# Performance work log

Measured on AMD Instinct MI355X. Metric: run time of the kernel, lower is better.

The kernel has to match this reference:

```python
import jax, jax.numpy as jnp
import numpy as np

N = 40000   # input nodes
M = 40000   # output nodes
DEG = 16    # fixed degree -> row_splits = arange(M+1)*DEG
E = M * DEG
B = 2
C = 128     # out_channels == feature channels
H = 128     # hidden_dim
P = 3       # positional dim per node (in_channels)


def setup_inputs() -> dict:
    key = jax.random.key(0)
    k = jax.random.split(key, 8)
    x_in = jax.random.normal(k[0], (N, P), dtype=jnp.float32)
    x_out = jax.random.normal(k[1], (M, P), dtype=jnp.float32)
    in_features = jax.random.normal(k[2], (B, N, C), dtype=jnp.float32)
    neighbor_idx = jax.random.randint(k[3], (E,), 0, N)
    row_splits = jnp.arange(M + 1, dtype=jnp.int32) * DEG
    W1 = jax.random.normal(k[4], (2 * P, H), dtype=jnp.float32) / np.sqrt(2 * P)
    b1 = jnp.zeros((H,), dtype=jnp.float32)
    W2 = jax.random.normal(k[5], (H, C), dtype=jnp.float32) / np.sqrt(H)
    b2 = jnp.zeros((C,), dtype=jnp.float32)
    return {"x_in": x_in, "x_out": x_out, "in_features": in_features,
            "neighbor_idx": neighbor_idx, "row_splits": row_splits,
            "W1": W1, "b1": b1, "W2": W2, "b2": b2}


def reference(x_in, x_out, in_features, neighbor_idx, row_splits, W1, b1, W2, b2):
    e = neighbor_idx.shape[0]
    m = row_splits.shape[0] - 1
    num_reps = row_splits[1:] - row_splits[:-1]               # [M]
    rep_feats = x_in[neighbor_idx]                            # [E, P] gather source coords
    gathered = in_features[:, neighbor_idx]                   # [B, E, C]
    self_feats = jnp.repeat(x_out, num_reps, axis=0, total_repeat_length=e)  # [E, P]
    agg = jnp.concatenate([rep_feats, self_feats], axis=1)    # [E, 2P]
    h = jax.nn.gelu(agg @ W1 + b1, approximate=False)         # torch.nn.GELU = exact erf gelu
    msg = h @ W2 + b2                                         # [E, C]
    weighted = msg[None, :, :] * gathered                     # [B, E, C]
    seg_ids = jnp.repeat(jnp.arange(m), num_reps, total_repeat_length=e)      # [E]
    sums = jax.ops.segment_sum(jnp.transpose(weighted, (1, 0, 2)), seg_ids, num_segments=m)  # [M, B, C]
    counts = jnp.maximum(num_reps, 1).astype(sums.dtype)      # segment_csr 'mean'
    out = sums / counts[:, None, None]                        # [M, B, C]
    return jnp.transpose(out, (1, 0, 2))                      # [B, M, C]
```

## Files before the change

kernel.cpp:

```cpp
#include <hip/hip_runtime.h>
#include <hip/hip_bf16.h>

#define CC 128
#define HH 128
#define NB 8

typedef __attribute__((ext_vector_type(8))) _Float16 half8;
typedef __attribute__((ext_vector_type(2))) _Float16 half2v;
typedef __attribute__((ext_vector_type(2))) __fp16   fp16x2;
typedef __attribute__((ext_vector_type(4))) float f32x4;

union H2U { half2v h; fp16x2 g; unsigned int u; };

__device__ __forceinline__ unsigned int pkrtz(float a, float b) {
    H2U v; v.g = __builtin_amdgcn_cvt_pkrtz(a, b); return v.u;
}

__device__ __forceinline__ float gelu_f(float x) {
    float x2 = x * x;
    float t  = fmaf(0.044715f, x2, 1.0f);
    float a  = x * t;
    float e  = __builtin_amdgcn_exp2f(a * 2.3022092f);
    float r  = __builtin_amdgcn_rcpf(e + 1.0f);
    return fmaf(-x, r, x);
}

__global__ __launch_bounds__(256)
void f32_to_f16_kernel(const float* __restrict__ in,
                       _Float16* __restrict__ out, long n8) {
    long i = (long)blockIdx.x * blockDim.x + threadIdx.x;
    const long stride = (long)gridDim.x * blockDim.x;
    for (; i < n8; i += stride) {
        const float4* p = reinterpret_cast<const float4*>(in) + i * 2;
        float4 a = p[0], b = p[1];
        half8 o;
        o[0] = (_Float16)a.x; o[1] = (_Float16)a.y;
        o[2] = (_Float16)a.z; o[3] = (_Float16)a.w;
        o[4] = (_Float16)b.x; o[5] = (_Float16)b.y;
        o[6] = (_Float16)b.z; o[7] = (_Float16)b.w;
        *reinterpret_cast<half8*>(out + i * 8) = o;
    }
}

template<bool F16G>
__global__ __launch_bounds__(512, 4)
void nmlp_kernel(const float* __restrict__ x_in,
                 const float* __restrict__ x_out,
                 const float* __restrict__ in_feat,
                 const _Float16* __restrict__ gws,
                 const int* __restrict__ nbr,
                 const int* __restrict__ row_splits,
                 const float* __restrict__ W1,
                 const float* __restrict__ b1,
                 const float* __restrict__ W2,
                 const float* __restrict__ b2,
                 float* __restrict__ out,
                 int N, int M)
{
    __shared__ __align__(16) char hb[NB * 16 * 256];
    __shared__ __align__(16) char msgb[NB * 16 * 256];
    __shared__ __align__(16) char aggb[NB * 16 * 16];

    const int tid  = threadIdx.x;
    const int lane = tid & 63;
    const int wave = tid >> 6;
    const int cbase = wave * 16;
    const int l15  = lane & 15;
    const int kgrp = lane >> 4;

    half8 w1frag;
    #pragma unroll
    for (int i = 0; i < 8; ++i) {
        int k = kgrp*8 + i;
        w1frag[i] = (k < 6) ? (_Float16)W1[k*HH + cbase + l15] : (_Float16)0.f;
    }
    half8 bfrag[4];
    #pragma unroll
    for (int kb = 0; kb < 4; ++kb)
        #pragma unroll
        for (int i = 0; i < 8; ++i) {
            int k = kb*32 + kgrp*8 + i;
            bfrag[kb][i] = (_Float16)W2[k*CC + cbase + l15];
        }
    float b1v[4], b2v[4];
    #pragma unroll
    for (int i = 0; i < 4; ++i) {
        b1v[i] = b1[cbase + kgrp*4 + i];
        b2v[i] = b2[cbase + kgrp*4 + i];
    }

    const _Float16* g0p = gws;
    const _Float16* g1p = gws + (size_t)N * CC;
    const float* f0p = in_feat;
    const float* f1p = in_feat + (size_t)N * CC;

    const int arow_off = l15 * 256;
    const int aswz = (l15 & 7) << 4;
    const int wcol_off = (cbase + kgrp*4) * 2;

    const int bb     = lane >> 5;
    const int ehalf  = (lane >> 4) & 1;
    const int cchunk = lane & 15;
    const _Float16* gpb = bb ? g1p : g0p;

    const int ngroups = (M + NB - 1) / NB;
    for (int g = blockIdx.x; g < ngroups; g += gridDim.x) {
        const int m0 = g * NB;
        const int mw = m0 + wave;

        int sW = 0, dgv = 0;
        if (mw < M) { sW = row_splits[mw]; dgv = row_splits[mw+1] - sW; }
        const int dgs = __builtin_amdgcn_readfirstlane(dgv);
        int ids8[8];
        if (dgs == 16 && ((sW & 3) == 0)) {
            const int4 ia = *reinterpret_cast<const int4*>(nbr + sW + ehalf*8);
            const int4 ib = *reinterpret_cast<const int4*>(nbr + sW + ehalf*8 + 4);
            ids8[0]=ia.x; ids8[1]=ia.y; ids8[2]=ia.z; ids8[3]=ia.w;
            ids8[4]=ib.x; ids8[5]=ib.y; ids8[6]=ib.z; ids8[7]=ib.w;
        } else {
            #pragma unroll
            for (int e8 = 0; e8 < 8; ++e8) {
                const int e = ehalf*8 + e8;
                ids8[e8] = (e < dgs) ? nbr[sW + e] : 0;
            }
        }
        uint4 gv[8];
        if (F16G) {
            const _Float16* gcp = gpb + cchunk*8;
            #pragma unroll
            for (int e8 = 0; e8 < 8; ++e8)
                gv[e8] = *reinterpret_cast<const uint4*>(
                    gcp + (size_t)ids8[e8]*CC);
        }

        if (tid < NB*16) {
            const int r = tid >> 4, e = tid & 15;
            const int m = m0 + r;
            int id = 0; int dg = 0;
            if (m < M) { int s = row_splits[m]; dg = row_splits[m+1] - s;
                         if (e < dg) id = nbr[s + e]; }
            const bool valid = (m < M) && (e < dg);
            float a0=0.f,a1=0.f,a2=0.f,a3=0.f,a4=0.f,a5=0.f;
            if (valid) {
                a0 = x_in[id*3+0]; a1 = x_in[id*3+1]; a2 = x_in[id*3+2];
                a3 = x_out[m*3+0]; a4 = x_out[m*3+1]; a5 = x_out[m*3+2];
            }
            uint4 pk;
            pk.x = pkrtz(a0, a1);
            pk.y = pkrtz(a2, a3);
            pk.z = pkrtz(a4, a5);
            pk.w = 0u;
            *reinterpret_cast<uint4*>(&aggb[tid*16]) = pk;
        }
        __syncthreads();

        #pragma unroll
        for (int r = 0; r < NB; ++r) {
            half8 af = *reinterpret_cast<const half8*>(&aggb[(r*16 + l15)*16]);
            f32x4 pa = {b1v[0], b1v[1], b1v[2], b1v[3]};
            pa = __builtin_amdgcn_mfma_f32_16x16x32_f16(w1frag, af, pa, 0, 0, 0);
            float g0 = gelu_f(pa[0]);
            float g1 = gelu_f(pa[1]);
            float g2 = gelu_f(pa[2]);
            float g3 = gelu_f(pa[3]);
            uint2 w = make_uint2(pkrtz(g0, g1), pkrtz(g2, g3));
            *reinterpret_cast<uint2*>(
                hb + r*4096 + l15*256 + (wcol_off ^ aswz)) = w;
        }
        __syncthreads();

        #pragma unroll
        for (int r = 0; r < NB; ++r) {
            f32x4 a = {b2v[0], b2v[1], b2v[2], b2v[3]};
            const char* base = hb + r*4096 + arow_off;
            #pragma unroll
            for (int kb = 0; kb < 4; ++kb) {
                half8 hf = *reinterpret_cast<const half8*>(
                    base + ((kb*64 + kgrp*16) ^ aswz));
                a = __builtin_amdgcn_mfma_f32_16x16x32_f16(bfrag[kb], hf, a, 0, 0, 0);
            }
            uint2 w = make_uint2(pkrtz(a[0], a[1]), pkrtz(a[2], a[3]));
            *reinterpret_cast<uint2*>(
                msgb + r*4096 + l15*256 + (wcol_off ^ aswz)) = w;
        }
        __syncthreads();

        if (mw < M) {
            half2v o0 = {0,0}, o1 = {0,0}, o2 = {0,0}, o3 = {0,0};
            const char* mbase = msgb + wave*4096;
            if (dgs == 16) {
                #pragma unroll
                for (int e8 = 0; e8 < 8; ++e8) {
                    const int e = ehalf*8 + e8;
                    const uint4 mv = *reinterpret_cast<const uint4*>(
                        mbase + e*256 + ((cchunk*16) ^ ((e & 7) << 4)));
                    const uint4 gvv = F16G ? gv[e8] : uint4{0,0,0,0};
                    uint4 gq = gvv;
                    if (!F16G) {
                        const float* fp = bb ? f1p : f0p;
                        const float4* q = reinterpret_cast<const float4*>(
                            fp + (size_t)ids8[e8]*CC + cchunk*8);
                        float4 qa = q[0], qb = q[1];
                        gq.x = pkrtz(qa.x, qa.y); gq.y = pkrtz(qa.z, qa.w);
                        gq.z = pkrtz(qb.x, qb.y); gq.w = pkrtz(qb.z, qb.w);
                    }
                    H2U ma, ga;
                    ma.u = mv.x; ga.u = gq.x; o0 += ma.h * ga.h;
                    ma.u = mv.y; ga.u = gq.y; o1 += ma.h * ga.h;
                    ma.u = mv.z; ga.u = gq.z; o2 += ma.h * ga.h;
                    ma.u = mv.w; ga.u = gq.w; o3 += ma.h * ga.h;
                }
            } else {
                #pragma unroll
                for (int e8 = 0; e8 < 8; ++e8) {
                    const int e = ehalf*8 + e8;
                    if (e < dgs) {
                        const uint4 mv = *reinterpret_cast<const uint4*>(
                            mbase + e*256 + ((cchunk*16) ^ ((e & 7) << 4)));
                        uint4 gq;
                        if (F16G) gq = gv[e8];
                        else {
                            const float* fp = bb ? f1p : f0p;
                            const float4* q = reinterpret_cast<const float4*>(
                                fp + (size_t)ids8[e8]*CC + cchunk*8);
                            float4 qa = q[0], qb = q[1];
                            gq.x = pkrtz(qa.x, qa.y); gq.y = pkrtz(qa.z, qa.w);
                            gq.z = pkrtz(qb.x, qb.y); gq.w = pkrtz(qb.z, qb.w);
                        }
                        H2U ma, ga;
                        ma.u = mv.x; ga.u = gq.x; o0 += ma.h * ga.h;
                        ma.u = mv.y; ga.u = gq.y; o1 += ma.h * ga.h;
                        ma.u = mv.z; ga.u = gq.z; o2 += ma.h * ga.h;
                        ma.u = mv.w; ga.u = gq.w; o3 += ma.h * ga.h;
                    }
                }
            }
            H2U u0, u1, u2, u3, p;
            u0.h = o0; u1.h = o1; u2.h = o2; u3.h = o3;
            p.u = (unsigned int)__shfl_xor((int)u0.u, 16); u0.h += p.h;
            p.u = (unsigned int)__shfl_xor((int)u1.u, 16); u1.h += p.h;
            p.u = (unsigned int)__shfl_xor((int)u2.u, 16); u2.h += p.h;
            p.u = (unsigned int)__shfl_xor((int)u3.u, 16); u3.h += p.h;
            if (ehalf == 0) {
                const float invd = (dgs == 16) ? 0.0625f
                                 : 1.f / (float)(dgs > 0 ? dgs : 1);
                float* op = out + (size_t)bb*M*CC + (size_t)mw*CC + cchunk*8;
                float4 v0 = {(float)u0.h[0]*invd, (float)u0.h[1]*invd,
                             (float)u1.h[0]*invd, (float)u1.h[1]*invd};
                float4 v1 = {(float)u2.h[0]*invd, (float)u2.h[1]*invd,
                             (float)u3.h[0]*invd, (float)u3.h[1]*invd};
                *reinterpret_cast<float4*>(op)     = v0;
                *reinterpret_cast<float4*>(op + 4) = v1;
            }
        }
        __syncthreads();
    }
}

extern "C" void kernel_launch(void* const* d_in, const int* in_sizes, int n_in,
                              void* d_out, int out_size, void* d_ws, size_t ws_size,
                              hipStream_t stream) {
    const float* x_in    = (const float*)d_in[0];
    const float* x_out   = (const float*)d_in[1];
    const float* in_feat = (const float*)d_in[2];
    const int*   nbr     = (const int*)d_in[3];
    const int*   rs      = (const int*)d_in[4];
    const float* W1      = (const float*)d_in[5];
    const float* b1      = (const float*)d_in[6];
    const float* W2      = (const float*)d_in[7];
    const float* b2      = (const float*)d_in[8];
    float* out = (float*)d_out;

    const int N = in_sizes[0] / 3;
    const int M = in_sizes[1] / 3;

    const int ngroups = (M + NB - 1) / NB;
    int grid = ngroups < 512 ? ngroups : 512;

    const size_t nfeat = (size_t)2 * N * CC;
    const bool use_f16 = (ws_size >= nfeat * sizeof(_Float16)) &&
                         (nfeat % 8 == 0);
    if (use_f16) {
        const long n8 = (long)(nfeat / 8);
        int cgrid = (int)((n8 + 255) / 256);
        if (cgrid > 4096) cgrid = 4096;
        f32_to_f16_kernel<<<cgrid, 256, 0, stream>>>(
            in_feat, (_Float16*)d_ws, n8);
        nmlp_kernel<true><<<grid, 512, 0, stream>>>(
            x_in, x_out, in_feat, (const _Float16*)d_ws,
            nbr, rs, W1, b1, W2, b2, out, N, M);
    } else {
        nmlp_kernel<false><<<grid, 512, 0, stream>>>(
            x_in, x_out, in_feat, nullptr,
            nbr, rs, W1, b1, W2, b2, out, N, M);
    }
}
```

Before: 90.23 us.

## Halve block to four waves, each computing two column tiles; drop trailing barrier

Shrinks the node group per block from 8 to 4 output nodes and the block from 512 to 256 threads. Each wave now computes two 16-column tiles of both MLP layers instead of one, reusing each loaded A fragment across two MFMAs. The grid cap rises to 1024 blocks and the end-of-iteration __syncthreads is removed, since the barriers at the start of the next iteration already order the shared-memory reuse. The aim is smaller LDS per block, more resident blocks and less synchronisation, at the cost of doubled weight-fragment registers per thread.

```diff
diff --git a/kernel.cpp b/kernel.cpp
--- a/kernel.cpp
+++ b/kernel.cpp
@@ -3,7 +3,7 @@
 
 #define CC 128
 #define HH 128
-#define NB 8
+#define NB 4
 
 typedef __attribute__((ext_vector_type(8))) _Float16 half8;
 typedef __attribute__((ext_vector_type(2))) _Float16 half2v;
@@ -43,7 +43,7 @@
 }
 
 template<bool F16G>
-__global__ __launch_bounds__(512, 4)
+__global__ __launch_bounds__(256, 4)
 void nmlp_kernel(const float* __restrict__ x_in,
                  const float* __restrict__ x_out,
                  const float* __restrict__ in_feat,
@@ -64,29 +64,33 @@
     const int tid  = threadIdx.x;
     const int lane = tid & 63;
     const int wave = tid >> 6;
-    const int cbase = wave * 16;
     const int l15  = lane & 15;
     const int kgrp = lane >> 4;
 
-    half8 w1frag;
+    half8 w1frag[2];
+    half8 bfrag[2][4];
+    float b1v[2][4], b2v[2][4];
     #pragma unroll
-    for (int i = 0; i < 8; ++i) {
-        int k = kgrp*8 + i;
-        w1frag[i] = (k < 6) ? (_Float16)W1[k*HH + cbase + l15] : (_Float16)0.f;
-    }
-    half8 bfrag[4];
-    #pragma unroll
-    for (int kb = 0; kb < 4; ++kb)
+    for (int tt = 0; tt < 2; ++tt) {
+        const int cb = (2*wave + tt) * 16;
         #pragma unroll
         for (int i = 0; i < 8; ++i) {
-            int k = kb*32 + kgrp*8 + i;
-            bfrag[kb][i] = (_Float16)W2[k*CC + cbase + l15];
-        }
-    float b1v[4], b2v[4];
-    #pragma unroll
-    for (int i = 0; i < 4; ++i) {
-        b1v[i] = b1[cbase + kgrp*4 + i];
-        b2v[i] = b2[cbase + kgrp*4 + i];
+            int k = kgrp*8 + i;
+            w1frag[tt][i] = (k < 6) ? (_Float16)W1[k*HH + cb + l15]
+                                    : (_Float16)0.f;
+        }
+        #pragma unroll
+        for (int kb = 0; kb < 4; ++kb)
+            #pragma unroll
+            for (int i = 0; i < 8; ++i) {
+                int k = kb*32 + kgrp*8 + i;
+                bfrag[tt][kb][i] = (_Float16)W2[k*CC + cb + l15];
+            }
+        #pragma unroll
+        for (int i = 0; i < 4; ++i) {
+            b1v[tt][i] = b1[cb + kgrp*4 + i];
+            b2v[tt][i] = b2[cb + kgrp*4 + i];
+        }
     }
 
     const _Float16* g0p = gws;
@@ -94,9 +98,8 @@
     const float* f0p = in_feat;
     const float* f1p = in_feat + (size_t)N * CC;
 
-    const int arow_off = l15 * 256;
     const int aswz = (l15 & 7) << 4;
-    const int wcol_off = (cbase + kgrp*4) * 2;
+    const int wrow_off = l15 * 256;
 
     const int bb     = lane >> 5;
     const int ehalf  = (lane >> 4) & 1;
@@ -157,31 +160,41 @@
         #pragma unroll
         for (int r = 0; r < NB; ++r) {
             half8 af = *reinterpret_cast<const half8*>(&aggb[(r*16 + l15)*16]);
-            f32x4 pa = {b1v[0], b1v[1], b1v[2], b1v[3]};
-            pa = __builtin_amdgcn_mfma_f32_16x16x32_f16(w1frag, af, pa, 0, 0, 0);
-            float g0 = gelu_f(pa[0]);
-            float g1 = gelu_f(pa[1]);
-            float g2 = gelu_f(pa[2]);
-            float g3 = gelu_f(pa[3]);
-            uint2 w = make_uint2(pkrtz(g0, g1), pkrtz(g2, g3));
-            *reinterpret_cast<uint2*>(
-                hb + r*4096 + l15*256 + (wcol_off ^ aswz)) = w;
+            #pragma unroll
+            for (int tt = 0; tt < 2; ++tt) {
+                f32x4 pa = {b1v[tt][0], b1v[tt][1], b1v[tt][2], b1v[tt][3]};
+                pa = __builtin_amdgcn_mfma_f32_16x16x32_f16(w1frag[tt], af, pa, 0, 0, 0);
+                float g0 = gelu_f(pa[0]);
+                float g1 = gelu_f(pa[1]);
+                float g2 = gelu_f(pa[2]);
+                float g3 = gelu_f(pa[3]);
+                const int c0 = (2*wave + tt)*16 + kgrp*4;
+                uint2 w = make_uint2(pkrtz(g0, g1), pkrtz(g2, g3));
+                *reinterpret_cast<uint2*>(
+                    hb + r*4096 + wrow_off + ((c0*2) ^ aswz)) = w;
+            }
         }
         __syncthreads();
 
         #pragma unroll
         for (int r = 0; r < NB; ++r) {
-            f32x4 a = {b2v[0], b2v[1], b2v[2], b2v[3]};
-            const char* base = hb + r*4096 + arow_off;
+            f32x4 a0c = {b2v[0][0], b2v[0][1], b2v[0][2], b2v[0][3]};
+            f32x4 a1c = {b2v[1][0], b2v[1][1], b2v[1][2], b2v[1][3]};
+            const char* base = hb + r*4096 + wrow_off;
             #pragma unroll
             for (int kb = 0; kb < 4; ++kb) {
                 half8 hf = *reinterpret_cast<const half8*>(
                     base + ((kb*64 + kgrp*16) ^ aswz));
-                a = __builtin_amdgcn_mfma_f32_16x16x32_f16(bfrag[kb], hf, a, 0, 0, 0);
-            }
-            uint2 w = make_uint2(pkrtz(a[0], a[1]), pkrtz(a[2], a[3]));
+                a0c = __builtin_amdgcn_mfma_f32_16x16x32_f16(bfrag[0][kb], hf, a0c, 0, 0, 0);
+                a1c = __builtin_amdgcn_mfma_f32_16x16x32_f16(bfrag[1][kb], hf, a1c, 0, 0, 0);
+            }
+            const int c0 = 2*wave*16 + kgrp*4;
+            uint2 w0 = make_uint2(pkrtz(a0c[0], a0c[1]), pkrtz(a0c[2], a0c[3]));
+            uint2 w1 = make_uint2(pkrtz(a1c[0], a1c[1]), pkrtz(a1c[2], a1c[3]));
             *reinterpret_cast<uint2*>(
-                msgb + r*4096 + l15*256 + (wcol_off ^ aswz)) = w;
+                msgb + r*4096 + wrow_off + ((c0*2) ^ aswz)) = w0;
+            *reinterpret_cast<uint2*>(
+                msgb + r*4096 + wrow_off + (((c0+16)*2) ^ aswz)) = w1;
         }
         __syncthreads();
 
@@ -194,8 +207,7 @@
                     const int e = ehalf*8 + e8;
                     const uint4 mv = *reinterpret_cast<const uint4*>(
                         mbase + e*256 + ((cchunk*16) ^ ((e & 7) << 4)));
-                    const uint4 gvv = F16G ? gv[e8] : uint4{0,0,0,0};
-                    uint4 gq = gvv;
+                    uint4 gq = F16G ? gv[e8] : uint4{0,0,0,0};
                     if (!F16G) {
                         const float* fp = bb ? f1p : f0p;
                         const float4* q = reinterpret_cast<const float4*>(
@@ -253,7 +265,6 @@
                 *reinterpret_cast<float4*>(op + 4) = v1;
             }
         }
-        __syncthreads();
     }
 }
 
@@ -275,7 +286,7 @@
     const int M = in_sizes[1] / 3;
 
     const int ngroups = (M + NB - 1) / NB;
-    int grid = ngroups < 512 ? ngroups : 512;
+    int grid = ngroups < 1024 ? ngroups : 1024;
 
     const size_t nfeat = (size_t)2 * N * CC;
     const bool use_f16 = (ws_size >= nfeat * sizeof(_Float16)) &&
@@ -286,11 +297,11 @@
         if (cgrid > 4096) cgrid = 4096;
         f32_to_f16_kernel<<<cgrid, 256, 0, stream>>>(
             in_feat, (_Float16*)d_ws, n8);
-        nmlp_kernel<true><<<grid, 512, 0, stream>>>(
+        nmlp_kernel<true><<<grid, 256, 0, stream>>>(
             x_in, x_out, in_feat, (const _Float16*)d_ws,
             nbr, rs, W1, b1, W2, b2, out, N, M);
     } else {
-        nmlp_kernel<false><<<grid, 512, 0, stream>>>(
+        nmlp_kernel<false><<<grid, 256, 0, stream>>>(
             x_in, x_out, in_feat, nullptr,
             nbr, rs, W1, b1, W2, b2, out, N, M);
     }
```

Result: faster. 87.46 us (-3.1%).

## Halve nodes per block, split batch across waves, raise occupancy, drop trailing barrier

Applied to the files above, without the earlier changes.

Each block now processes 4 output nodes instead of 8. Each wave is mapped to one (node, batch) pair, and each lane gathers 4 edges instead of 8, with an extra cross-lane shuffle stage to reduce over the four edge groups. This halves per-thread gather registers. That allows launch bounds targeting 6 blocks per CU and a larger grid, so more memory loads are in flight to hide gather latency. The end-of-iteration __syncthreads is removed; this relies on the two intermediate barriers to protect the shared buffers, and the smaller groups mean more MLP-phase barriers per node.

```diff
diff --git a/kernel.cpp b/kernel.cpp
--- a/kernel.cpp
+++ b/kernel.cpp
@@ -3,7 +3,7 @@
 
 #define CC 128
 #define HH 128
-#define NB 8
+#define NB 4
 
 typedef __attribute__((ext_vector_type(8))) _Float16 half8;
 typedef __attribute__((ext_vector_type(2))) _Float16 half2v;
@@ -43,7 +43,7 @@
 }
 
 template<bool F16G>
-__global__ __launch_bounds__(512, 4)
+__global__ __launch_bounds__(512, 6)
 void nmlp_kernel(const float* __restrict__ x_in,
                  const float* __restrict__ x_out,
                  const float* __restrict__ in_feat,
@@ -82,55 +82,52 @@
             int k = kb*32 + kgrp*8 + i;
             bfrag[kb][i] = (_Float16)W2[k*CC + cbase + l15];
         }
-    float b1v[4], b2v[4];
-    #pragma unroll
-    for (int i = 0; i < 4; ++i) {
-        b1v[i] = b1[cbase + kgrp*4 + i];
-        b2v[i] = b2[cbase + kgrp*4 + i];
-    }
+    f32x4 b1v = {b1[cbase + kgrp*4 + 0], b1[cbase + kgrp*4 + 1],
+                 b1[cbase + kgrp*4 + 2], b1[cbase + kgrp*4 + 3]};
+    f32x4 b2v = {b2[cbase + kgrp*4 + 0], b2[cbase + kgrp*4 + 1],
+                 b2[cbase + kgrp*4 + 2], b2[cbase + kgrp*4 + 3]};
 
     const _Float16* g0p = gws;
     const _Float16* g1p = gws + (size_t)N * CC;
     const float* f0p = in_feat;
     const float* f1p = in_feat + (size_t)N * CC;
 
-    const int arow_off = l15 * 256;
     const int aswz = (l15 & 7) << 4;
+    const int wrow_off = l15 * 256;
     const int wcol_off = (cbase + kgrp*4) * 2;
 
-    const int bb     = lane >> 5;
-    const int ehalf  = (lane >> 4) & 1;
+    const int nd2b   = wave & 3;
+    const int bb     = wave >> 2;
+    const int egrp   = lane >> 4;
     const int cchunk = lane & 15;
-    const _Float16* gpb = bb ? g1p : g0p;
+    const _Float16* gpb = (bb ? g1p : g0p) + cchunk*8;
+    const float*    fpb = (bb ? f1p : f0p) + cchunk*8;
 
     const int ngroups = (M + NB - 1) / NB;
     for (int g = blockIdx.x; g < ngroups; g += gridDim.x) {
         const int m0 = g * NB;
-        const int mw = m0 + wave;
+        const int mw = m0 + nd2b;
 
         int sW = 0, dgv = 0;
         if (mw < M) { sW = row_splits[mw]; dgv = row_splits[mw+1] - sW; }
         const int dgs = __builtin_amdgcn_readfirstlane(dgv);
-        int ids8[8];
+        int ids4[4];
         if (dgs == 16 && ((sW & 3) == 0)) {
-            const int4 ia = *reinterpret_cast<const int4*>(nbr + sW + ehalf*8);
-            const int4 ib = *reinterpret_cast<const int4*>(nbr + sW + ehalf*8 + 4);
-            ids8[0]=ia.x; ids8[1]=ia.y; ids8[2]=ia.z; ids8[3]=ia.w;
-            ids8[4]=ib.x; ids8[5]=ib.y; ids8[6]=ib.z; ids8[7]=ib.w;
+            const int4 ia = *reinterpret_cast<const int4*>(nbr + sW + egrp*4);
+            ids4[0]=ia.x; ids4[1]=ia.y; ids4[2]=ia.z; ids4[3]=ia.w;
         } else {
             #pragma unroll
-            for (int e8 = 0; e8 < 8; ++e8) {
-                const int e = ehalf*8 + e8;
-                ids8[e8] = (e < dgs) ? nbr[sW + e] : 0;
-            }
-        }
-        uint4 gv[8];
+            for (int e4 = 0; e4 < 4; ++e4) {
+                const int e = egrp*4 + e4;
+                ids4[e4] = (e < dgs) ? nbr[sW + e] : 0;
+            }
+        }
+        uint4 gv[4];
         if (F16G) {
-            const _Float16* gcp = gpb + cchunk*8;
             #pragma unroll
-            for (int e8 = 0; e8 < 8; ++e8)
-                gv[e8] = *reinterpret_cast<const uint4*>(
-                    gcp + (size_t)ids8[e8]*CC);
+            for (int e4 = 0; e4 < 4; ++e4)
+                gv[e4] = *reinterpret_cast<const uint4*>(
+                    gpb + (size_t)ids4[e4]*CC);
         }
 
         if (tid < NB*16) {
@@ -157,7 +154,7 @@
         #pragma unroll
         for (int r = 0; r < NB; ++r) {
             half8 af = *reinterpret_cast<const half8*>(&aggb[(r*16 + l15)*16]);
-            f32x4 pa = {b1v[0], b1v[1], b1v[2], b1v[3]};
+            f32x4 pa = b1v;
             pa = __builtin_amdgcn_mfma_f32_16x16x32_f16(w1frag, af, pa, 0, 0, 0);
             float g0 = gelu_f(pa[0]);
             float g1 = gelu_f(pa[1]);
@@ -165,14 +162,14 @@
             float g3 = gelu_f(pa[3]);
             uint2 w = make_uint2(pkrtz(g0, g1), pkrtz(g2, g3));
             *reinterpret_cast<uint2*>(
-                hb + r*4096 + l15*256 + (wcol_off ^ aswz)) = w;
+                hb + r*4096 + wrow_off + (wcol_off ^ aswz)) = w;
         }
         __syncthreads();
 
         #pragma unroll
         for (int r = 0; r < NB; ++r) {
-            f32x4 a = {b2v[0], b2v[1], b2v[2], b2v[3]};
-            const char* base = hb + r*4096 + arow_off;
+            f32x4 a = b2v;
+            const char* base = hb + r*4096 + wrow_off;
             #pragma unroll
             for (int kb = 0; kb < 4; ++kb) {
                 half8 hf = *reinterpret_cast<const half8*>(
@@ -181,25 +178,23 @@
             }
             uint2 w = make_uint2(pkrtz(a[0], a[1]), pkrtz(a[2], a[3]));
             *reinterpret_cast<uint2*>(
-                msgb + r*4096 + l15*256 + (wcol_off ^ aswz)) = w;
+                msgb + r*4096 + wrow_off + (wcol_off ^ aswz)) = w;
         }
         __syncthreads();
 
         if (mw < M) {
             half2v o0 = {0,0}, o1 = {0,0}, o2 = {0,0}, o3 = {0,0};
-            const char* mbase = msgb + wave*4096;
+            const char* mbase = msgb + nd2b*4096;
             if (dgs == 16) {
                 #pragma unroll
-                for (int e8 = 0; e8 < 8; ++e8) {
-                    const int e = ehalf*8 + e8;
+                for (int e4 = 0; e4 < 4; ++e4) {
+                    const int e = egrp*4 + e4;
                     const uint4 mv = *reinterpret_cast<const uint4*>(
                         mbase + e*256 + ((cchunk*16) ^ ((e & 7) << 4)));
-                    const uint4 gvv = F16G ? gv[e8] : uint4{0,0,0,0};
-                    uint4 gq = gvv;
+                    uint4 gq = F16G ? gv[e4] : uint4{0,0,0,0};
                     if (!F16G) {
-                        const float* fp = bb ? f1p : f0p;
                         const float4* q = reinterpret_cast<const float4*>(
-                            fp + (size_t)ids8[e8]*CC + cchunk*8);
+                            fpb + (size_t)ids4[e4]*CC);
                         float4 qa = q[0], qb = q[1];
                         gq.x = pkrtz(qa.x, qa.y); gq.y = pkrtz(qa.z, qa.w);
                         gq.z = pkrtz(qb.x, qb.y); gq.w = pkrtz(qb.z, qb.w);
@@ -212,17 +207,16 @@
                 }
             } else {
                 #pragma unroll
-                for (int e8 = 0; e8 < 8; ++e8) {
-                    const int e = ehalf*8 + e8;
+                for (int e4 = 0; e4 < 4; ++e4) {
+                    const int e = egrp*4 + e4;
                     if (e < dgs) {
                         const uint4 mv = *reinterpret_cast<const uint4*>(
                             mbase + e*256 + ((cchunk*16) ^ ((e & 7) << 4)));
                         uint4 gq;
-                        if (F16G) gq = gv[e8];
+                        if (F16G) gq = gv[e4];
                         else {
-                            const float* fp = bb ? f1p : f0p;
                             const float4* q = reinterpret_cast<const float4*>(
-                                fp + (size_t)ids8[e8]*CC + cchunk*8);
+                                fpb + (size_t)ids4[e4]*CC);
                             float4 qa = q[0], qb = q[1];
                             gq.x = pkrtz(qa.x, qa.y); gq.y = pkrtz(qa.z, qa.w);
                             gq.z = pkrtz(qb.x, qb.y); gq.w = pkrtz(qb.z, qb.w);
@@ -241,7 +235,11 @@
             p.u = (unsigned int)__shfl_xor((int)u1.u, 16); u1.h += p.h;
             p.u = (unsigned int)__shfl_xor((int)u2.u, 16); u2.h += p.h;
             p.u = (unsigned int)__shfl_xor((int)u3.u, 16); u3.h += p.h;
-            if (ehalf == 0) {
+            p.u = (unsigned int)__shfl_xor((int)u0.u, 32); u0.h += p.h;
+            p.u = (unsigned int)__shfl_xor((int)u1.u, 32); u1.h += p.h;
+            p.u = (unsigned int)__shfl_xor((int)u2.u, 32); u2.h += p.h;
+            p.u = (unsigned int)__shfl_xor((int)u3.u, 32); u3.h += p.h;
+            if (egrp == 0) {
                 const float invd = (dgs == 16) ? 0.0625f
                                  : 1.f / (float)(dgs > 0 ? dgs : 1);
                 float* op = out + (size_t)bb*M*CC + (size_t)mw*CC + cchunk*8;
@@ -253,7 +251,6 @@
                 *reinterpret_cast<float4*>(op + 4) = v1;
             }
         }
-        __syncthreads();
     }
 }
 
@@ -275,7 +272,7 @@
     const int M = in_sizes[1] / 3;
 
     const int ngroups = (M + NB - 1) / NB;
-    int grid = ngroups < 512 ? ngroups : 512;
+    int grid = ngroups < 1024 ? ngroups : 1024;
 
     const size_t nfeat = (size_t)2 * N * CC;
     const bool use_f16 = (ws_size >= nfeat * sizeof(_Float16)) &&
```

Result: slower. 126.5 us (+40.2%).
